# Optimization experiments

Measured on AMD Instinct MI355X. Metric: run time of the kernel, lower is better.

The kernel has to match this reference:

```python
import jax, jax.numpy as jnp
import numpy as np

EPS = 1e-5

def _fake_quant(w, axis):
    # symmetric int8 fake-quant with straight-through estimator
    s = jnp.max(jnp.abs(w), axis=axis, keepdims=True) / 127.0 + 1e-8
    q = jnp.clip(jnp.round(w / s), -127.0, 127.0) * s
    return w + jax.lax.stop_gradient(q - w)

def _qconv1x1(x, w, b):
    # x: [B, C_in, Q, H, W]; w: [C_out, C_in] (1x1 kernel); weight fake-quantized
    wq = _fake_quant(w, axis=1)
    return jnp.einsum('bcqhw,oc->boqhw', x, wq) + b[None, :, None, None, None]

def setup_inputs() -> dict:
    key = jax.random.key(0)
    ks = jax.random.split(key, 12)
    B, C, Q, H, W = 8, 256, 4, 40, 40
    x = jax.random.normal(ks[0], (B, C, Q, H, W), dtype=jnp.float32)
    scale = 1.0 / np.sqrt(C)
    Wq = jax.random.normal(ks[1], (C, C), dtype=jnp.float32) * scale
    Wk = jax.random.normal(ks[2], (C, C), dtype=jnp.float32) * scale
    Wv = jax.random.normal(ks[3], (C, C), dtype=jnp.float32) * scale
    Wp = jax.random.normal(ks[4], (C, C), dtype=jnp.float32) * scale
    bq = jnp.zeros((C,), jnp.float32)
    bk = jnp.zeros((C,), jnp.float32)
    bv = jnp.zeros((C,), jnp.float32)
    bp = jnp.zeros((C,), jnp.float32)
    gamma = jnp.ones((C,), jnp.float32)
    beta = jnp.zeros((C,), jnp.float32)
    return {"x": x, "Wq": Wq, "bq": bq, "Wk": Wk, "bk": bk,
            "Wv": Wv, "bv": bv, "Wp": Wp, "bp": bp,
            "gamma": gamma, "beta": beta}

def reference(x, Wq, bq, Wk, bk, Wv, bv, Wp, bp, gamma, beta):
    B, C, Q, H, W = x.shape
    q = _qconv1x1(x, Wq, bq)
    k = _qconv1x1(x, Wk, bk)
    v = _qconv1x1(x, Wv, bv)
    # per-rotation channel attention: [B, Q=4, C, H*W]
    qh = q.reshape(B, C, Q, H * W).transpose(0, 2, 1, 3)
    kh = k.reshape(B, C, Q, H * W).transpose(0, 2, 1, 3)
    vh = v.reshape(B, C, Q, H * W).transpose(0, 2, 1, 3)
    scale = 1.0 / jnp.sqrt(jnp.float32(C // 4))
    attn = jnp.einsum('bqcn,bqdn->bqcd', qh, kh) * scale  # [B,4,C,C]
    attn = jax.nn.softmax(attn, axis=-1)
    out = jnp.einsum('bqcd,bqdn->bqcn', attn, vh)  # [B,4,C,HW]
    out = out.transpose(0, 2, 1, 3).reshape(B, C, Q, H, W)
    out = _qconv1x1(out, Wp, bp)
    # IQBN: per-channel batchnorm with int8 fake-quantized gamma
    mean = jnp.mean(out, axis=(0, 2, 3, 4), keepdims=True)
    var = jnp.var(out, axis=(0, 2, 3, 4), keepdims=True)
    g = _fake_quant(gamma, axis=None)[None, :, None, None, None]
    b = beta[None, :, None, None, None]
    out = (out - mean) * jax.lax.rsqrt(var + EPS) * g + b
    return out
```

## Files before the change

### kernel.cpp

```cpp
#include <hip/hip_runtime.h>
#include <math.h>

#define BB 8
#define CCH 256
#define QQ 4
#define NN 1600
#define BQN 32
#define SP 51200
#define EPSF 1e-5f

typedef __attribute__((ext_vector_type(8))) short bf16x8;
typedef __attribute__((ext_vector_type(4))) float f32x4;

static __device__ inline ushort f2bf(float f) {
  union { float f; unsigned u; } v; v.f = f;
  return (ushort)((v.u + 0x7fffu + ((v.u >> 16) & 1u)) >> 16);
}
static __device__ inline float bf2f(ushort u) {
  union { unsigned u; float f; } v; v.u = ((unsigned)u) << 16;
  return v.f;
}
static __device__ inline bf16x8 ldg8(const ushort* p) {
  return *(const bf16x8*)p;
}
static __device__ inline void gld16(const ushort* g, ushort* l) {
  __builtin_amdgcn_global_load_lds(
      (const __attribute__((address_space(1))) unsigned int*)g,
      (__attribute__((address_space(3))) unsigned int*)l, 16, 0, 0);
}

__global__ void quant_weights_kernel(const float* Wq, const float* Wk,
                                     const float* Wv, const float* Wp,
                                     const float* gamma,
                                     ushort* wq, ushort* wk, ushort* wvT, ushort* wp,
                                     ushort* wqT, ushort* wkT, ushort* wpT,
                                     float* gq, float* r,
                                     float* m_acc, float* v_acc) {
  __shared__ float red[256];
  int blk = blockIdx.x;
  int tid = threadIdx.x;
  if (blk < 1024) {
    int mat = blk >> 8;
    int row = blk & 255;
    const float* W = (mat == 0) ? Wq : (mat == 1) ? Wk : (mat == 2) ? Wv : Wp;
    float w = W[row * 256 + tid];
    red[tid] = fabsf(w);
    __syncthreads();
    for (int s = 128; s > 0; s >>= 1) {
      if (tid < s) red[tid] = fmaxf(red[tid], red[tid + s]);
      __syncthreads();
    }
    float s = red[0] / 127.0f + 1e-8f;
    float q = fminf(fmaxf(rintf(w / s), -127.0f), 127.0f) * s;
    ushort qb = f2bf(q);
    if (mat == 0)      { wq[row * 256 + tid] = qb; wqT[tid * 256 + row] = qb; }
    else if (mat == 1) { wk[row * 256 + tid] = qb; wkT[tid * 256 + row] = qb; }
    else if (mat == 2) { wvT[tid * 256 + row] = qb; }
    else               { wp[row * 256 + tid] = qb; wpT[tid * 256 + row] = qb; }
  } else {
    float g = gamma[tid];
    red[tid] = fabsf(g);
    __syncthreads();
    for (int s = 128; s > 0; s >>= 1) {
      if (tid < s) red[tid] = fmaxf(red[tid], red[tid + s]);
      __syncthreads();
    }
    float s = red[0] / 127.0f + 1e-8f;
    gq[tid] = fminf(fmaxf(rintf(g / s), -127.0f), 127.0f) * s;
    for (int i = tid; i < BQN * 256; i += 256) r[i] = 0.f;
    m_acc[tid] = 0.f;
    v_acc[tid] = 0.f;
  }
}

__global__ __launch_bounds__(256)
void prep_kernel(const float* __restrict__ x, ushort* __restrict__ xb,
                 ushort* __restrict__ xT, float* __restrict__ r) {
  int bqi = blockIdx.z, b = bqi >> 2, q = bqi & 3;
  int s0 = blockIdx.x * 64, c0 = blockIdx.y * 64;
  __shared__ ushort lT[64 * 66];
  int tid = threadIdx.x;
  int c = tid >> 2, nch = (tid & 3) * 16;
  const float* xp = x + ((size_t)(b * CCH + c0 + c) * QQ + q) * NN + s0 + nch;
  union { ushort u[16]; int4 v[2]; } nb;
  float s = 0.f;
#pragma unroll
  for (int j = 0; j < 4; j++) {
    float4 f = ((const float4*)xp)[j];
    ushort b0 = f2bf(f.x), b1 = f2bf(f.y), b2 = f2bf(f.z), b3 = f2bf(f.w);
    s += bf2f(b0) + bf2f(b1) + bf2f(b2) + bf2f(b3);
    nb.u[j * 4 + 0] = b0;
    nb.u[j * 4 + 1] = b1;
    nb.u[j * 4 + 2] = b2;
    nb.u[j * 4 + 3] = b3;
    lT[c * 66 + nch + j * 4 + 0] = b0;
    lT[c * 66 + nch + j * 4 + 1] = b1;
    lT[c * 66 + nch + j * 4 + 2] = b2;
    lT[c * 66 + nch + j * 4 + 3] = b3;
  }
  ushort* xbp = xb + (size_t)bqi * (CCH * NN) + (size_t)(c0 + c) * NN + s0 + nch;
  *(int4*)xbp = nb.v[0];
  *((int4*)xbp + 1) = nb.v[1];
  s += __shfl_down(s, 2);
  s += __shfl_down(s, 1);
  if ((tid & 3) == 0) atomicAdd(&r[bqi * 256 + c0 + c], s);
  __syncthreads();
  int n = tid >> 2, cch = (tid & 3) * 16;
  union { ushort u[16]; int4 v[2]; } o;
#pragma unroll
  for (int i = 0; i < 16; i++) o.u[i] = lT[(cch + i) * 66 + n];
  ushort* dst = xT + (size_t)(bqi * NN + s0 + n) * CCH + c0 + cch;
  *(int4*)dst = o.v[0];
  *((int4*)dst + 1) = o.v[1];
}

__global__ __launch_bounds__(256)
void gram_uv_kernel(const ushort* __restrict__ xb, ushort* __restrict__ Gh,
                    ushort* __restrict__ Gl,
                    const ushort* __restrict__ wqT, const ushort* __restrict__ wkT,
                    const float* __restrict__ r, float* __restrict__ u,
                    float* __restrict__ vv) {
  __shared__ __align__(16) float lCw_s[2304];
  __shared__ float rs[256];
  int t = blockIdx.x, z = blockIdx.y;
  int tid = threadIdx.x;
  if (t == 10) {
    rs[tid] = r[z * 256 + tid];
    __syncthreads();
    float su = 0.f, sv = 0.f;
    for (int i = 0; i < 256; i++) {
      float rv = rs[i];
      su += bf2f(wqT[i * 256 + tid]) * rv;
      sv += bf2f(wkT[i * 256 + tid]) * rv;
    }
    u[z * 256 + tid] = su;
    vv[z * 256 + tid] = sv;
    return;
  }
  int ty = (t >= 4) + (t >= 7) + (t >= 9);
  int base = ty * 4 - (ty * (ty - 1)) / 2;
  int tx = ty + (t - base);
  int mBase = ty * 64, nBase = tx * 64;
  bool offd = (tx != ty);
  int wave = tid >> 6, lane = tid & 63;
  int wm = wave >> 1, wn = wave & 1;
  int col = lane & 15, quad = lane >> 4;
  const ushort* X = xb + (size_t)z * (CCH * NN);
  const ushort* pA0 = X + (size_t)(mBase + wm * 32 + col) * NN + quad * 8;
  const ushort* pA1 = pA0 + (size_t)16 * NN;
  const ushort* pB0 = X + (size_t)(nBase + wn * 32 + col) * NN + quad * 8;
  const ushort* pB1 = pB0 + (size_t)16 * NN;
  f32x4 acc[2][2];
#pragma unroll
  for (int i = 0; i < 2; i++)
#pragma unroll
    for (int j = 0; j < 2; j++) acc[i][j] = (f32x4){0.f, 0.f, 0.f, 0.f};
#pragma unroll 2
  for (int kk = 0; kk < NN; kk += 32) {
    bf16x8 a0 = ldg8(pA0 + kk), a1 = ldg8(pA1 + kk);
    bf16x8 b0 = ldg8(pB0 + kk), b1 = ldg8(pB1 + kk);
    acc[0][0] = __builtin_amdgcn_mfma_f32_16x16x32_bf16(a0, b0, acc[0][0], 0, 0, 0);
    acc[0][1] = __builtin_amdgcn_mfma_f32_16x16x32_bf16(a0, b1, acc[0][1], 0, 0, 0);
    acc[1][0] = __builtin_amdgcn_mfma_f32_16x16x32_bf16(a1, b0, acc[1][0], 0, 0, 0);
    acc[1][1] = __builtin_amdgcn_mfma_f32_16x16x32_bf16(a1, b1, acc[1][1], 0, 0, 0);
  }
  float* lCw = lCw_s + wave * 576;
#pragma unroll
  for (int i = 0; i < 2; i++) {
#pragma unroll
    for (int j = 0; j < 2; j++)
#pragma unroll
      for (int rg = 0; rg < 4; rg++)
        lCw[(quad * 4 + rg) * 36 + j * 16 + col] = acc[i][j][rg];
    int mrow0 = mBase + wm * 32 + i * 16;
    int nW = nBase + wn * 32;
    int rr = lane >> 2, cc = (lane & 3) * 8;
    union { ushort u[8]; int4 v; } oh, ol;
#pragma unroll
    for (int t8 = 0; t8 < 8; t8++) {
      float vfl = lCw[rr * 36 + cc + t8];
      ushort hh = f2bf(vfl);
      oh.u[t8] = hh;
      ol.u[t8] = f2bf(vfl - bf2f(hh));
    }
    size_t off = (size_t)z * 65536 + (size_t)(mrow0 + rr) * 256 + nW + cc;
    *(int4*)(Gh + off) = oh.v;
    *(int4*)(Gl + off) = ol.v;
    if (offd) {
      int nn = lane >> 1, mh = (lane & 1) * 8;
      union { ushort u[8]; int4 v; } th, tl;
#pragma unroll
      for (int t8 = 0; t8 < 8; t8++) {
        float vfl = lCw[(mh + t8) * 36 + nn];
        ushort hh = f2bf(vfl);
        th.u[t8] = hh;
        tl.u[t8] = f2bf(vfl - bf2f(hh));
      }
      size_t offT = (size_t)z * 65536 + (size_t)(nW + nn) * 256 + mrow0 + mh;
      *(int4*)(Gh + offT) = th.v;
      *(int4*)(Gl + offT) = tl.v;
    }
  }
}

__global__ __launch_bounds__(512)
void spk_kernel(const ushort* __restrict__ wq, const ushort* __restrict__ Gh,
                const ushort* __restrict__ Gl, const ushort* __restrict__ wk,
                const float* __restrict__ ug, const float* __restrict__ vg,
                const float* __restrict__ bqv, const float* __restrict__ bkv,
                const float* __restrict__ bvv,
                ushort* __restrict__ P, float* __restrict__ pb) {
  __shared__ __align__(16) char smem[33792];
  ushort* M1h_l = (ushort*)smem;
  ushort* M1l_l = M1h_l + 8448;
  int z = blockIdx.y, mBase = blockIdx.x * 32;
  int tid = threadIdx.x, w = tid >> 6, lane = tid & 63;
  int col = lane & 15, quad = lane >> 4;
  const ushort* Ghz = Gh + (size_t)z * 65536;
  const ushort* Glz = Gl + (size_t)z * 65536;

  f32x4 acc[2][2];
#pragma unroll
  for (int i = 0; i < 2; i++)
#pragma unroll
    for (int j = 0; j < 2; j++) acc[i][j] = (f32x4){0.f, 0.f, 0.f, 0.f};
  {
    const ushort* pA0 = wq + (size_t)(mBase + col) * 256 + quad * 8;
    const ushort* pA1 = pA0 + 16 * 256;
    const ushort* pH0 = Ghz + (size_t)(w * 32 + col) * 256 + quad * 8;
    const ushort* pH1 = pH0 + 16 * 256;
    const ushort* pL0 = Glz + (size_t)(w * 32 + col) * 256 + quad * 8;
    const ushort* pL1 = pL0 + 16 * 256;
#pragma unroll
    for (int kk = 0; kk < 256; kk += 32) {
      bf16x8 a0 = ldg8(pA0 + kk), a1 = ldg8(pA1 + kk);
      bf16x8 h0 = ldg8(pH0 + kk), h1 = ldg8(pH1 + kk);
      bf16x8 l0 = ldg8(pL0 + kk), l1 = ldg8(pL1 + kk);
      acc[0][0] = __builtin_amdgcn_mfma_f32_16x16x32_bf16(a0, h0, acc[0][0], 0, 0, 0);
      acc[0][0] = __builtin_amdgcn_mfma_f32_16x16x32_bf16(a0, l0, acc[0][0], 0, 0, 0);
      acc[0][1] = __builtin_amdgcn_mfma_f32_16x16x32_bf16(a0, h1, acc[0][1], 0, 0, 0);
      acc[0][1] = __builtin_amdgcn_mfma_f32_16x16x32_bf16(a0, l1, acc[0][1], 0, 0, 0);
      acc[1][0] = __builtin_amdgcn_mfma_f32_16x16x32_bf16(a1, h0, acc[1][0], 0, 0, 0);
      acc[1][0] = __builtin_amdgcn_mfma_f32_16x16x32_bf16(a1, l0, acc[1][0], 0, 0, 0);
      acc[1][1] = __builtin_amdgcn_mfma_f32_16x16x32_bf16(a1, h1, acc[1][1], 0, 0, 0);
      acc[1][1] = __builtin_amdgcn_mfma_f32_16x16x32_bf16(a1, l1, acc[1][1], 0, 0, 0);
    }
  }
#pragma unroll
  for (int i = 0; i < 2; i++)
#pragma unroll
    for (int j = 0; j < 2; j++)
#pragma unroll
      for (int rg = 0; rg < 4; rg++) {
        int ml = i * 16 + quad * 4 + rg;
        int cg = w * 32 + j * 16 + col;
        float vfl = acc[i][j][rg];
        ushort hh = f2bf(vfl);
        M1h_l[ml * 264 + cg] = hh;
        M1l_l[ml * 264 + cg] = f2bf(vfl - bf2f(hh));
      }
  __syncthreads();

  f32x4 acc2[2][2];
#pragma unroll
  for (int i = 0; i < 2; i++)
#pragma unroll
    for (int j = 0; j < 2; j++) acc2[i][j] = (f32x4){0.f, 0.f, 0.f, 0.f};
  {
    const ushort* pW0 = wk + (size_t)(w * 32 + col) * 256 + quad * 8;
    const ushort* pW1 = pW0 + 16 * 256;
#pragma unroll
    for (int kk = 0; kk < 256; kk += 32) {
      bf16x8 ah0 = *(const bf16x8*)&M1h_l[(col) * 264 + kk + quad * 8];
      bf16x8 ah1 = *(const bf16x8*)&M1h_l[(16 + col) * 264 + kk + quad * 8];
      bf16x8 al0 = *(const bf16x8*)&M1l_l[(col) * 264 + kk + quad * 8];
      bf16x8 al1 = *(const bf16x8*)&M1l_l[(16 + col) * 264 + kk + quad * 8];
      bf16x8 b0 = ldg8(pW0 + kk), b1 = ldg8(pW1 + kk);
      acc2[0][0] = __builtin_amdgcn_mfma_f32_16x16x32_bf16(ah0, b0, acc2[0][0], 0, 0, 0);
      acc2[0][0] = __builtin_amdgcn_mfma_f32_16x16x32_bf16(al0, b0, acc2[0][0], 0, 0, 0);
      acc2[0][1] = __builtin_amdgcn_mfma_f32_16x16x32_bf16(ah0, b1, acc2[0][1], 0, 0, 0);
      acc2[0][1] = __builtin_amdgcn_mfma_f32_16x16x32_bf16(al0, b1, acc2[0][1], 0, 0, 0);
      acc2[1][0] = __builtin_amdgcn_mfma_f32_16x16x32_bf16(ah1, b0, acc2[1][0], 0, 0, 0);
      acc2[1][0] = __builtin_amdgcn_mfma_f32_16x16x32_bf16(al1, b0, acc2[1][0], 0, 0, 0);
      acc2[1][1] = __builtin_amdgcn_mfma_f32_16x16x32_bf16(ah1, b1, acc2[1][1], 0, 0, 0);
      acc2[1][1] = __builtin_amdgcn_mfma_f32_16x16x32_bf16(al1, b1, acc2[1][1], 0, 0, 0);
    }
  }
  __syncthreads();

  float* Sb = (float*)smem;
  float bkc[2], vvc[2];
#pragma unroll
  for (int j = 0; j < 2; j++) {
    int cg = w * 32 + j * 16 + col;
    bkc[j] = bkv[cg];
    vvc[j] = vg[z * 256 + cg];
  }
#pragma unroll
  for (int i = 0; i < 2; i++)
#pragma unroll
    for (int rg = 0; rg < 4; rg++) {
      int ml = i * 16 + quad * 4 + rg;
      int rglob = mBase + ml;
      float uu = ug[z * 256 + rglob];
      float bqc = bqv[rglob];
#pragma unroll
      for (int j = 0; j < 2; j++)
        Sb[ml * 260 + w * 32 + j * 16 + col] =
            0.125f * (acc2[i][j][rg] + uu * bkc[j] + bqc * vvc[j] + 1600.0f * bqc * bkc[j]);
    }
  __syncthreads();

  float4 bv4 = *(const float4*)(bvv + lane * 4);
#pragma unroll
  for (int rr4 = 0; rr4 < 4; ++rr4) {
    int rloc = w * 4 + rr4;
    f32x4 sv = *(const f32x4*)&Sb[rloc * 260 + lane * 4];
    float x0 = sv[0], x1 = sv[1], x2 = sv[2], x3 = sv[3];
    float m = fmaxf(fmaxf(x0, x1), fmaxf(x2, x3));
#pragma unroll
    for (int s = 32; s > 0; s >>= 1) m = fmaxf(m, __shfl_xor(m, s));
    float e0 = expf(x0 - m), e1 = expf(x1 - m), e2 = expf(x2 - m), e3 = expf(x3 - m);
    float t = e0 + e1 + e2 + e3;
#pragma unroll
    for (int s = 32; s > 0; s >>= 1) t += __shfl_xor(t, s);
    float is = 1.0f / t;
    float p0 = e0 * is, p1 = e1 * is, p2 = e2 * is, p3 = e3 * is;
    union { ushort u[4]; uint2 v; } o;
    o.u[0] = f2bf(p0); o.u[1] = f2bf(p1); o.u[2] = f2bf(p2); o.u[3] = f2bf(p3);
    *(uint2*)(P + (size_t)z * 65536 + (size_t)(mBase + rloc) * 256 + lane * 4) = o.v;
    float d = p0 * bv4.x + p1 * bv4.y + p2 * bv4.z + p3 * bv4.w;
#pragma unroll
    for (int s = 32; s > 0; s >>= 1) d += __shfl_xor(d, s);
    if (lane == 0) pb[z * 256 + mBase + rloc] = d;
  }
}

__global__ __launch_bounds__(512)
void pt_kernel(const ushort* __restrict__ P, const ushort* __restrict__ wvT,
               const ushort* __restrict__ wp,
               ushort* __restrict__ Tm, ushort* __restrict__ TmT) {
  __shared__ __align__(16) char smem[18432];
  ushort* N1b = (ushort*)smem;
  int z = blockIdx.y, cs = blockIdx.x * 32;
  int tid = threadIdx.x, w = tid >> 6, lane = tid & 63;
  int col = lane & 15, quad = lane >> 4;
  const ushort* Pz = P + (size_t)z * 65536;

  f32x4 acc[2][2];
#pragma unroll
  for (int i = 0; i < 2; i++)
#pragma unroll
    for (int j = 0; j < 2; j++) acc[i][j] = (f32x4){0.f, 0.f, 0.f, 0.f};
  {
    const ushort* pP0 = Pz + (size_t)(w * 32 + col) * 256 + quad * 8;
    const ushort* pP1 = pP0 + 16 * 256;
    const ushort* pV0 = wvT + (size_t)(cs + col) * 256 + quad * 8;
    const ushort* pV1 = pV0 + 16 * 256;
#pragma unroll
    for (int kk = 0; kk < 256; kk += 32) {
      bf16x8 a0 = ldg8(pP0 + kk), a1 = ldg8(pP1 + kk);
      bf16x8 b0 = ldg8(pV0 + kk), b1 = ldg8(pV1 + kk);
      acc[0][0] = __builtin_amdgcn_mfma_f32_16x16x32_bf16(a0, b0, acc[0][0], 0, 0, 0);
      acc[0][1] = __builtin_amdgcn_mfma_f32_16x16x32_bf16(a0, b1, acc[0][1], 0, 0, 0);
      acc[1][0] = __builtin_amdgcn_mfma_f32_16x16x32_bf16(a1, b0, acc[1][0], 0, 0, 0);
      acc[1][1] = __builtin_amdgcn_mfma_f32_16x16x32_bf16(a1, b1, acc[1][1], 0, 0, 0);
    }
  }
#pragma unroll
  for (int i = 0; i < 2; i++)
#pragma unroll
    for (int j = 0; j < 2; j++)
#pragma unroll
      for (int rg = 0; rg < 4; rg++) {
        int e = w * 32 + i * 16 + quad * 4 + rg;
        int cl = j * 16 + col;
        N1b[cl * 264 + e] = f2bf(acc[i][j][rg]);
      }
  __syncthreads();

  f32x4 acc2[2][2];
#pragma unroll
  for (int i = 0; i < 2; i++)
#pragma unroll
    for (int j = 0; j < 2; j++) acc2[i][j] = (f32x4){0.f, 0.f, 0.f, 0.f};
  {
    const ushort* pW0 = wp + (size_t)(w * 32 + col) * 256 + quad * 8;
    const ushort* pW1 = pW0 + 16 * 256;
#pragma unroll
    for (int kk = 0; kk < 256; kk += 32) {
      bf16x8 a0 = ldg8(pW0 + kk), a1 = ldg8(pW1 + kk);
      bf16x8 b0 = *(const bf16x8*)&N1b[(col) * 264 + kk + quad * 8];
      bf16x8 b1 = *(const bf16x8*)&N1b[(16 + col) * 264 + kk + quad * 8];
      acc2[0][0] = __builtin_amdgcn_mfma_f32_16x16x32_bf16(a0, b0, acc2[0][0], 0, 0, 0);
      acc2[0][1] = __builtin_amdgcn_mfma_f32_16x16x32_bf16(a0, b1, acc2[0][1], 0, 0, 0);
      acc2[1][0] = __builtin_amdgcn_mfma_f32_16x16x32_bf16(a1, b0, acc2[1][0], 0, 0, 0);
      acc2[1][1] = __builtin_amdgcn_mfma_f32_16x16x32_bf16(a1, b1, acc2[1][1], 0, 0, 0);
    }
  }
  __syncthreads();

  float* lCw = (float*)smem + w * 576;
#pragma unroll
  for (int i = 0; i < 2; i++) {
#pragma unroll
    for (int j = 0; j < 2; j++)
#pragma unroll
      for (int rg = 0; rg < 4; rg++)
        lCw[(quad * 4 + rg) * 36 + j * 16 + col] = acc2[i][j][rg];
    int oW = w * 32 + i * 16;
    int rr = lane >> 2, cc = (lane & 3) * 8;
    union { ushort u[8]; int4 v; } o;
#pragma unroll
    for (int t8 = 0; t8 < 8; t8++) o.u[t8] = f2bf(lCw[rr * 36 + cc + t8]);
    *(int4*)(Tm + (size_t)z * 65536 + (size_t)(oW + rr) * 256 + cs + cc) = o.v;
    int nn = lane >> 1, mh = (lane & 1) * 8;
    union { ushort u[8]; int4 v; } o2;
#pragma unroll
    for (int t8 = 0; t8 < 8; t8++) o2.u[t8] = f2bf(lCw[(mh + t8) * 36 + nn]);
    *(int4*)(TmT + (size_t)z * 65536 + (size_t)(cs + nn) * 256 + oW + mh) = o2.v;
  }
}

__global__ __launch_bounds__(256)
void dsq_kernel(const ushort* __restrict__ Tm, const ushort* __restrict__ Gh,
                const ushort* __restrict__ Gl, float* __restrict__ v_acc) {
  int z = blockIdx.z;
  int mBase = blockIdx.y * 64, nBase = blockIdx.x * 64;
  int tid = threadIdx.x, wave = tid >> 6, lane = tid & 63;
  int wm = wave >> 1, wn = wave & 1;
  int col = lane & 15, quad = lane >> 4;
  const ushort* Tz = Tm + (size_t)z * 65536;
  const ushort* Ghz = Gh + (size_t)z * 65536;
  const ushort* Glz = Gl + (size_t)z * 65536;
  const ushort* pA0 = Tz + (size_t)(mBase + wm * 32 + col) * 256 + quad * 8;
  const ushort* pA1 = pA0 + 16 * 256;
  const ushort* pH0 = Ghz + (size_t)(nBase + wn * 32 + col) * 256 + quad * 8;
  const ushort* pH1 = pH0 + 16 * 256;
  const ushort* pL0 = Glz + (size_t)(nBase + wn * 32 + col) * 256 + quad * 8;
  const ushort* pL1 = pL0 + 16 * 256;
  f32x4 acc[2][2];
#pragma unroll
  for (int i = 0; i < 2; i++)
#pragma unroll
    for (int j = 0; j < 2; j++) acc[i][j] = (f32x4){0.f, 0.f, 0.f, 0.f};
#pragma unroll
  for (int kk = 0; kk < 256; kk += 32) {
    bf16x8 a0 = ldg8(pA0 + kk), a1 = ldg8(pA1 + kk);
    bf16x8 h0 = ldg8(pH0 + kk), h1 = ldg8(pH1 + kk);
    bf16x8 l0 = ldg8(pL0 + kk), l1 = ldg8(pL1 + kk);
    acc[0][0] = __builtin_amdgcn_mfma_f32_16x16x32_bf16(a0, h0, acc[0][0], 0, 0, 0);
    acc[0][0] = __builtin_amdgcn_mfma_f32_16x16x32_bf16(a0, l0, acc[0][0], 0, 0, 0);
    acc[0][1] = __builtin_amdgcn_mfma_f32_16x16x32_bf16(a0, h1, acc[0][1], 0, 0, 0);
    acc[0][1] = __builtin_amdgcn_mfma_f32_16x16x32_bf16(a0, l1, acc[0][1], 0, 0, 0);
    acc[1][0] = __builtin_amdgcn_mfma_f32_16x16x32_bf16(a1, h0, acc[1][0], 0, 0, 0);
    acc[1][0] = __builtin_amdgcn_mfma_f32_16x16x32_bf16(a1, l0, acc[1][0], 0, 0, 0);
    acc[1][1] = __builtin_amdgcn_mfma_f32_16x16x32_bf16(a1, h1, acc[1][1], 0, 0, 0);
    acc[1][1] = __builtin_amdgcn_mfma_f32_16x16x32_bf16(a1, l1, acc[1][1], 0, 0, 0);
  }
#pragma unroll
  for (int i = 0; i < 2; i++) {
    int mr = mBase + wm * 32 + i * 16 + quad * 4;
#pragma unroll
    for (int rg = 0; rg < 4; rg++) {
      float p = 0.f;
#pragma unroll
      for (int j = 0; j < 2; j++)
        p += acc[i][j][rg] * bf2f(Tz[(mr + rg) * 256 + nBase + wn * 32 + j * 16 + col]);
      p += __shfl_down(p, 8);
      p += __shfl_down(p, 4);
      p += __shfl_down(p, 2);
      p += __shfl_down(p, 1);
      if (col == 0) atomicAdd(v_acc + mr + rg, p);
    }
  }
}

__global__ __launch_bounds__(256)
void bo_d1_kernel(const ushort* __restrict__ wpT, const ushort* __restrict__ TmT,
                  const float* __restrict__ pb, const float* __restrict__ rb,
                  const float* __restrict__ bp,
                  float* __restrict__ bo, float* __restrict__ m_acc,
                  float* __restrict__ v_acc) {
  int z = blockIdx.x, o = threadIdx.x;
  __shared__ float sp[256], sr[256];
  sp[o] = pb[z * 256 + o];
  sr[o] = rb[z * 256 + o];
  __syncthreads();
  float bv = bp[o], d1 = 0.f;
  const ushort* Tz = TmT + (size_t)z * 65536;
  for (int c = 0; c < 256; c++) {
    bv += bf2f(wpT[c * 256 + o]) * sp[c];
    d1 += bf2f(Tz[c * 256 + o]) * sr[c];
  }
  bo[z * 256 + o] = bv;
  atomicAdd(m_acc + o, d1 + 1600.0f * bv);
  atomicAdd(v_acc + o, 2.0f * bv * d1 + 1600.0f * bv * bv);
}

__global__ __launch_bounds__(256)
void final_kernel(const ushort* __restrict__ Tm, const ushort* __restrict__ xT,
                  const float* __restrict__ bo, const float* __restrict__ m_acc,
                  const float* __restrict__ v_acc, const float* __restrict__ gq,
                  const float* __restrict__ beta, float* __restrict__ out) {
  __shared__ __align__(16) char smem[32768];
  float* lC = (float*)smem;
  int z = blockIdx.z;
  int mBase = blockIdx.y * 128, nBase = blockIdx.x * 128;
  int tid = threadIdx.x, wave = tid >> 6, lane = tid & 63;
  int wm = wave >> 1, wn = wave & 1;
  int col = lane & 15, quad = lane >> 4;
  int srow = tid >> 2, skc = (tid & 3) * 8;
  const ushort* Az = Tm + (size_t)z * 65536;
  const ushort* Bz = xT + (size_t)z * (NN * 256);
  const ushort* gA  = Az + (size_t)(mBase + srow) * 256 + skc;
  const ushort* gA2 = gA + 64 * 256;
  int br1 = nBase + srow;      br1 = br1 < NN ? br1 : NN - 1;
  int br2 = nBase + 64 + srow; br2 = br2 < NN ? br2 : NN - 1;
  const ushort* gB  = Bz + (size_t)br1 * 256 + skc;
  const ushort* gB2 = Bz + (size_t)br2 * 256 + skc;
  ushort* sA1[2]; ushort* sA2[2]; ushort* sB1[2]; ushort* sB2[2];
#pragma unroll
  for (int b = 0; b < 2; b++) {
    ushort* lAb = (ushort*)(smem + b * 16384);
    ushort* lBb = (ushort*)(smem + b * 16384 + 8192);
    sA1[b] = &lAb[srow * 32 + skc];
    sA2[b] = &lAb[(64 + srow) * 32 + skc];
    sB1[b] = &lBb[srow * 32 + skc];
    sB2[b] = &lBb[(64 + srow) * 32 + skc];
  }
  f32x4 acc[4][4];
#pragma unroll
  for (int i = 0; i < 4; i++)
#pragma unroll
    for (int j = 0; j < 4; j++) acc[i][j] = (f32x4){0.f, 0.f, 0.f, 0.f};

  const int nIter = 8;
  gld16(gA, sA1[0]); gld16(gA2, sA2[0]); gld16(gB, sB1[0]); gld16(gB2, sB2[0]);
  for (int it = 0; it < nIter; ++it) {
    int cur = it & 1;
    __syncthreads();
    if (it + 1 < nIter) {
      int kt = (it + 1) << 5, nxt = cur ^ 1;
      gld16(gA + kt, sA1[nxt]); gld16(gA2 + kt, sA2[nxt]);
      gld16(gB + kt, sB1[nxt]); gld16(gB2 + kt, sB2[nxt]);
    }
    const ushort* lAc = (const ushort*)(smem + cur * 16384);
    const ushort* lBc = (const ushort*)(smem + cur * 16384 + 8192);
    bf16x8 af[4], bfr[4];
#pragma unroll
    for (int i = 0; i < 4; i++)
      af[i] = *(const bf16x8*)&lAc[(wm * 64 + i * 16 + col) * 32 + quad * 8];
#pragma unroll
    for (int j = 0; j < 4; j++)
      bfr[j] = *(const bf16x8*)&lBc[(wn * 64 + j * 16 + col) * 32 + quad * 8];
#pragma unroll
    for (int i = 0; i < 4; i++)
#pragma unroll
      for (int j = 0; j < 4; j++)
        acc[i][j] = __builtin_amdgcn_mfma_f32_16x16x32_bf16(af[i], bfr[j], acc[i][j], 0, 0, 0);
  }
  __syncthreads();
  float* lCw = lC + wave * 16 * 68;
  int mW = mBase + wm * 64, nW = nBase + wn * 64;
  int b = z >> 2, q = z & 3;
  const float inv = 1.0f / (float)SP;
#pragma unroll
  for (int i = 0; i < 4; i++) {
#pragma unroll
    for (int j = 0; j < 4; j++)
#pragma unroll
      for (int rg = 0; rg < 4; rg++)
        lCw[(quad * 4 + rg) * 68 + j * 16 + col] = acc[i][j][rg];
    int mrow0 = mW + i * 16;
    int rr = lane & 15, cc = lane >> 4;
    int n0 = nW + cc * 16;
    int o = mrow0 + rr;
    float bi = bo[(size_t)z * 256 + o];
    float mean = m_acc[o] * inv;
    float var = v_acc[o] * inv - mean * mean;
    float scl = rsqrtf(var + EPSF) * gq[o];
    float be = beta[o];
    if (n0 < NN) {
      float* C = out + (size_t)b * (CCH * QQ * NN)
               + (size_t)o * (QQ * NN) + (size_t)q * NN + n0;
#pragma unroll
      for (int v = 0; v < 4; v++) {
        float4 f;
        f.x = (lCw[rr * 68 + cc * 16 + v * 4 + 0] + bi - mean) * scl + be;
        f.y = (lCw[rr * 68 + cc * 16 + v * 4 + 1] + bi - mean) * scl + be;
        f.z = (lCw[rr * 68 + cc * 16 + v * 4 + 2] + bi - mean) * scl + be;
        f.w = (lCw[rr * 68 + cc * 16 + v * 4 + 3] + bi - mean) * scl + be;
        *(float4*)(C + v * 4) = f;
      }
    }
  }
}

extern "C" void kernel_launch(void* const* d_in, const int* in_sizes, int n_in,
                              void* d_out, int out_size, void* d_ws, size_t ws_size,
                              hipStream_t stream) {
  const float* x     = (const float*)d_in[0];
  const float* Wq    = (const float*)d_in[1];
  const float* bq    = (const float*)d_in[2];
  const float* Wk    = (const float*)d_in[3];
  const float* bk    = (const float*)d_in[4];
  const float* Wv    = (const float*)d_in[5];
  const float* bv    = (const float*)d_in[6];
  const float* Wp    = (const float*)d_in[7];
  const float* bp    = (const float*)d_in[8];
  const float* gamma = (const float*)d_in[9];
  const float* beta  = (const float*)d_in[10];
  float* out = (float*)d_out;

  ushort* h    = (ushort*)d_ws;
  ushort* wq   = h;
  ushort* wk   = wq + 65536;
  ushort* wp   = wk + 65536;
  ushort* wvT  = wp + 65536;
  ushort* wqT  = wvT + 65536;
  ushort* wkT  = wqT + 65536;
  ushort* wpT  = wkT + 65536;
  ushort* xb   = wpT + 65536;
  ushort* xT   = xb + (size_t)BQN * CCH * NN;
  ushort* Gh   = xT + (size_t)BQN * CCH * NN;
  ushort* Gl   = Gh + (size_t)BQN * 65536;
  ushort* P    = Gl + (size_t)BQN * 65536;
  ushort* Tm   = P + (size_t)BQN * 65536;
  ushort* TmT  = Tm + (size_t)BQN * 65536;
  float*  r    = (float*)(TmT + (size_t)BQN * 65536);
  float*  u    = r + 8192;
  float*  vv   = u + 8192;
  float*  pb   = vv + 8192;
  float*  bo   = pb + 8192;
  float*  m_acc = bo + 8192;
  float*  v_acc = m_acc + 256;
  float*  gq   = v_acc + 256;

  quant_weights_kernel<<<1025, 256, 0, stream>>>(Wq, Wk, Wv, Wp, gamma,
                                                 wq, wk, wvT, wp, wqT, wkT, wpT,
                                                 gq, r, m_acc, v_acc);
  prep_kernel<<<dim3(NN / 64, CCH / 64, BQN), 256, 0, stream>>>(x, xb, xT, r);
  gram_uv_kernel<<<dim3(11, BQN), 256, 0, stream>>>(xb, Gh, Gl, wqT, wkT, r, u, vv);
  spk_kernel<<<dim3(8, BQN), 512, 0, stream>>>(wq, Gh, Gl, wk, u, vv, bq, bk, bv, P, pb);
  pt_kernel<<<dim3(8, BQN), 512, 0, stream>>>(P, wvT, wp, Tm, TmT);
  dsq_kernel<<<dim3(4, 4, BQN), 256, 0, stream>>>(Tm, Gh, Gl, v_acc);
  bo_d1_kernel<<<BQN, 256, 0, stream>>>(wpT, TmT, pb, r, bp, bo, m_acc, v_acc);
  final_kernel<<<dim3(13, 2, BQN), 256, 0, stream>>>(Tm, xT, bo, m_acc, v_acc,
                                                     gq, beta, out);
}
```

Baseline: 293.9 us.

## Stage gram tiles through double-buffered LDS and remap block IDs for XCD locality

The gram kernel's main loop now loads each 64x32 A/B tile cooperatively from global memory into double-buffered shared memory with an async gld16 helper, then reads the MFMA fragments from LDS. This replaces per-wave direct global fragment loads with strided rows. Several kernels (gram, spk, pt, dsq) also remap linear block indices so that blocks sharing the same batch slice land on the same XCD (a lin&7 swizzle), aiming to improve L2 reuse. The cost is added __syncthreads per iteration and more shared memory. The remaps assume the grid sizes stay exactly as hard-coded.

```diff
diff --git a/kernel.cpp b/kernel.cpp
--- a/kernel.cpp
+++ b/kernel.cpp
@@ -120,9 +120,11 @@
                     const ushort* __restrict__ wqT, const ushort* __restrict__ wkT,
                     const float* __restrict__ r, float* __restrict__ u,
                     float* __restrict__ vv) {
-  __shared__ __align__(16) float lCw_s[2304];
+  __shared__ __align__(16) char smem[16384];
   __shared__ float rs[256];
-  int t = blockIdx.x, z = blockIdx.y;
+  int lin = blockIdx.x + 11 * blockIdx.y;
+  int nl = (lin & 7) * 44 + (lin >> 3);
+  int t = nl % 11, z = nl / 11;
   int tid = threadIdx.x;
   if (t == 10) {
     rs[tid] = r[z * 256 + tid];
@@ -146,25 +148,43 @@
   int wm = wave >> 1, wn = wave & 1;
   int col = lane & 15, quad = lane >> 4;
   const ushort* X = xb + (size_t)z * (CCH * NN);
-  const ushort* pA0 = X + (size_t)(mBase + wm * 32 + col) * NN + quad * 8;
-  const ushort* pA1 = pA0 + (size_t)16 * NN;
-  const ushort* pB0 = X + (size_t)(nBase + wn * 32 + col) * NN + quad * 8;
-  const ushort* pB1 = pB0 + (size_t)16 * NN;
+  const ushort* gA = X + (size_t)(mBase + (tid >> 2)) * NN + (tid & 3) * 8;
+  const ushort* gB = X + (size_t)(nBase + (tid >> 2)) * NN + (tid & 3) * 8;
   f32x4 acc[2][2];
 #pragma unroll
   for (int i = 0; i < 2; i++)
 #pragma unroll
     for (int j = 0; j < 2; j++) acc[i][j] = (f32x4){0.f, 0.f, 0.f, 0.f};
-#pragma unroll 2
-  for (int kk = 0; kk < NN; kk += 32) {
-    bf16x8 a0 = ldg8(pA0 + kk), a1 = ldg8(pA1 + kk);
-    bf16x8 b0 = ldg8(pB0 + kk), b1 = ldg8(pB1 + kk);
-    acc[0][0] = __builtin_amdgcn_mfma_f32_16x16x32_bf16(a0, b0, acc[0][0], 0, 0, 0);
-    acc[0][1] = __builtin_amdgcn_mfma_f32_16x16x32_bf16(a0, b1, acc[0][1], 0, 0, 0);
-    acc[1][0] = __builtin_amdgcn_mfma_f32_16x16x32_bf16(a1, b0, acc[1][0], 0, 0, 0);
-    acc[1][1] = __builtin_amdgcn_mfma_f32_16x16x32_bf16(a1, b1, acc[1][1], 0, 0, 0);
-  }
-  float* lCw = lCw_s + wave * 576;
+
+  const int nIter = NN / 32;
+  gld16(gA, (ushort*)smem + tid * 8);
+  gld16(gB, (ushort*)(smem + 4096) + tid * 8);
+  for (int it = 0; it < nIter; ++it) {
+    int cur = it & 1;
+    __syncthreads();
+    if (it + 1 < nIter) {
+      int kt = (it + 1) << 5;
+      char* bb = smem + (cur ^ 1) * 8192;
+      gld16(gA + kt, (ushort*)bb + tid * 8);
+      gld16(gB + kt, (ushort*)(bb + 4096) + tid * 8);
+    }
+    const ushort* lA = (const ushort*)(smem + cur * 8192);
+    const ushort* lB = lA + 2048;
+    bf16x8 af[2], bfr[2];
+#pragma unroll
+    for (int i = 0; i < 2; i++)
+      af[i] = *(const bf16x8*)&lA[(wm * 32 + i * 16 + col) * 32 + quad * 8];
+#pragma unroll
+    for (int j = 0; j < 2; j++)
+      bfr[j] = *(const bf16x8*)&lB[(wn * 32 + j * 16 + col) * 32 + quad * 8];
+#pragma unroll
+    for (int i = 0; i < 2; i++)
+#pragma unroll
+      for (int j = 0; j < 2; j++)
+        acc[i][j] = __builtin_amdgcn_mfma_f32_16x16x32_bf16(af[i], bfr[j], acc[i][j], 0, 0, 0);
+  }
+  __syncthreads();
+  float* lCw = (float*)smem + wave * 576;
 #pragma unroll
   for (int i = 0; i < 2; i++) {
 #pragma unroll
@@ -213,7 +233,9 @@
   __shared__ __align__(16) char smem[33792];
   ushort* M1h_l = (ushort*)smem;
   ushort* M1l_l = M1h_l + 8448;
-  int z = blockIdx.y, mBase = blockIdx.x * 32;
+  int lin = blockIdx.x + 8 * blockIdx.y;
+  int nl = (lin & 7) * 32 + (lin >> 3);
+  int mBase = (nl & 7) * 32, z = nl >> 3;
   int tid = threadIdx.x, w = tid >> 6, lane = tid & 63;
   int col = lane & 15, quad = lane >> 4;
   const ushort* Ghz = Gh + (size_t)z * 65536;
@@ -342,7 +364,9 @@
                ushort* __restrict__ Tm, ushort* __restrict__ TmT) {
   __shared__ __align__(16) char smem[18432];
   ushort* N1b = (ushort*)smem;
-  int z = blockIdx.y, cs = blockIdx.x * 32;
+  int lin = blockIdx.x + 8 * blockIdx.y;
+  int nl = (lin & 7) * 32 + (lin >> 3);
+  int cs = (nl & 7) * 32, z = nl >> 3;
   int tid = threadIdx.x, w = tid >> 6, lane = tid & 63;
   int col = lane & 15, quad = lane >> 4;
   const ushort* Pz = P + (size_t)z * 65536;
@@ -425,8 +449,9 @@
 __global__ __launch_bounds__(256)
 void dsq_kernel(const ushort* __restrict__ Tm, const ushort* __restrict__ Gh,
                 const ushort* __restrict__ Gl, float* __restrict__ v_acc) {
-  int z = blockIdx.z;
-  int mBase = blockIdx.y * 64, nBase = blockIdx.x * 64;
+  int lin = blockIdx.x + 4 * blockIdx.y + 16 * blockIdx.z;
+  int nl = (lin & 7) * 64 + (lin >> 3);
+  int mBase = (nl & 3) * 64, nBase = ((nl >> 2) & 3) * 64, z = nl >> 4;
   int tid = threadIdx.x, wave = tid >> 6, lane = tid & 63;
   int wm = wave >> 1, wn = wave & 1;
   int col = lane & 15, quad = lane >> 4;
```

New measurement: 264.9 us. 1.11x faster.
